# Kernel optimization log

Measured on AMD Instinct MI355X. Metric: run time of the kernel, lower is better.

The kernel has to match this reference:

```python
import jax, jax.numpy as jnp
import numpy as np

R = 3                 # corr_radius
STRIDE = 4
RES = (384, 512)      # model_resolution (H, W)
G = 2 * R + 1         # 7: support grid side


def setup_inputs() -> dict:
    key = jax.random.key(0)
    ks = jax.random.split(key, 16)
    B, S, N, C = 1, 8, 1024, 128
    H0, W0 = RES[0] // STRIDE, RES[1] // STRIDE  # 96, 128
    inp = {}
    for i in range(4):
        h, w = H0 >> i, W0 >> i
        inp[f"fmaps{i}"] = jax.random.normal(ks[i], (B, S, C, h, w), jnp.float32)
        inp[f"track{i}"] = jax.random.normal(ks[4 + i], (B, G * G, N, C), jnp.float32)
    inp["coords"] = jax.random.uniform(ks[8], (B, S, N, 2), jnp.float32) * jnp.asarray([W0 - 1.0, H0 - 1.0], jnp.float32)
    inp["vis"] = jax.random.normal(ks[9], (B, S, N, 1), jnp.float32)
    inp["conf"] = jax.random.normal(ks[10], (B, S, N, 1), jnp.float32)
    r2 = G * G
    inp["w1"] = jax.random.normal(ks[11], (r2 * r2, 384), jnp.float32) * (1.0 / np.sqrt(r2 * r2))
    inp["b1"] = jnp.zeros((384,), jnp.float32)
    inp["w2"] = jax.random.normal(ks[12], (384, 256), jnp.float32) * (1.0 / np.sqrt(384))
    inp["b2"] = jnp.zeros((256,), jnp.float32)
    inp["time_emb"] = jax.random.normal(ks[13], (1, S, 1110), jnp.float32) * 0.02
    return inp


def bilinear_sample(fmap, x, y):
    """fmap: (BT, C, H, W); x, y: (BT, M) pixel coords. Border padding, align_corners=True
    (matches torch grid_sample as used by co-tracker's bilinear_sampler)."""
    BT, C, H, W = fmap.shape
    x0f = jnp.floor(x)
    y0f = jnp.floor(y)
    wx = (x - x0f)[:, None, :]
    wy = (y - y0f)[:, None, :]
    x0 = jnp.clip(x0f.astype(jnp.int32), 0, W - 1)
    x1 = jnp.clip(x0f.astype(jnp.int32) + 1, 0, W - 1)
    y0 = jnp.clip(y0f.astype(jnp.int32), 0, H - 1)
    y1 = jnp.clip(y0f.astype(jnp.int32) + 1, 0, H - 1)
    flat = fmap.reshape(BT, C, H * W)

    def g(yi, xi):
        idx = (yi * W + xi)[:, None, :]  # (BT, 1, M)
        return jnp.take_along_axis(flat, idx, axis=2)  # (BT, C, M)

    return (g(y0, x0) * (1 - wx) * (1 - wy) + g(y0, x1) * wx * (1 - wy)
            + g(y1, x0) * (1 - wx) * wy + g(y1, x1) * wx * wy)


def posenc(x, min_deg=0, max_deg=10):
    scales = jnp.asarray([2.0 ** i for i in range(min_deg, max_deg)], x.dtype)
    xb = (x[..., None, :] * scales[:, None]).reshape(x.shape[:-1] + (-1,))
    four = jnp.sin(jnp.concatenate([xb, xb + 0.5 * jnp.pi], axis=-1))
    return jnp.concatenate([x, four], axis=-1)


def reference(fmaps0, fmaps1, fmaps2, fmaps3, track0, track1, track2, track3,
              coords, vis, conf, w1, b1, w2, b2, time_emb):
    B, S, N, _ = coords.shape
    fps = [fmaps0, fmaps1, fmaps2, fmaps3]
    tps = [track0, track1, track2, track3]
    d = jnp.linspace(-R, R, G)
    xoff, yoff = jnp.meshgrid(d, d, indexing='ij')  # (7,7): rows = x offset, cols = y offset

    embs = []
    for lvl in range(4):
        fm = fps[lvl]
        C, H, W = fm.shape[2], fm.shape[3], fm.shape[4]
        c = coords.reshape(B * S, N, 1, 1, 2) / (2.0 ** lvl)
        x = c[..., 0] + xoff          # (B*S, N, 7, 7)
        y = c[..., 1] + yoff
        M = N * G * G
        sampled = bilinear_sample(fm.reshape(B * S, C, H, W), x.reshape(B * S, M), y.reshape(B * S, M))
        corr_feat = sampled.reshape(B, S, C, N, G, G).transpose(0, 1, 3, 4, 5, 2)  # (B,S,N,7,7,C)
        track = tps[lvl].reshape(B, G, G, N, C).transpose(0, 3, 1, 2, 4)           # (B,N,7,7,C)
        vol = jnp.einsum('btnhwc,bnijc->btnhwij', corr_feat, track)                # (B,S,N,7,7,7,7)
        h = jax.nn.gelu(vol.reshape(B * S * N, G * G * G * G) @ w1 + b1, approximate=False)
        embs.append(h @ w2 + b2)
    corr_embs = jnp.concatenate(embs, axis=-1).reshape(B, S, N, -1)  # (B,S,N,1024)

    rel_f = jnp.pad(coords[:, :-1] - coords[:, 1:], ((0, 0), (0, 1), (0, 0), (0, 0)))
    rel_b = jnp.pad(coords[:, 1:] - coords[:, :-1], ((0, 0), (1, 0), (0, 0), (0, 0)))
    scale = jnp.asarray([RES[1], RES[0]], jnp.float32) / STRIDE
    rel_emb = posenc(jnp.concatenate([rel_f / scale, rel_b / scale], axis=-1))  # (B,S,N,84)

    x = jnp.concatenate([vis, conf, corr_embs, rel_emb], axis=-1)  # (B,S,N,1110)
    x = x.transpose(0, 2, 1, 3).reshape(B * N, S, -1) + time_emb
    return x.reshape(B, N, S, -1)
```

## Files before the change

kernel.cpp:

```cpp
#include <hip/hip_runtime.h>
#include <math.h>


#define SN 8
#define NN 1024
#define CC 128
#define K1P2 2752
#define H1 384
#define H2 256
#define DOUT 1110

typedef short bf16x8 __attribute__((ext_vector_type(8)));
typedef short s16x4 __attribute__((ext_vector_type(4)));
typedef float f32x4 __attribute__((ext_vector_type(4)));

__device__ inline unsigned short f2b(float x) {
    union { float f; unsigned u; } v; v.f = x;
    unsigned r = v.u + 0x7FFFu + ((v.u >> 16) & 1u);
    return (unsigned short)(r >> 16);
}
__device__ inline float b2f(unsigned short u) {
    union { unsigned u; float f; } v; v.u = (unsigned)u << 16; return v.f;
}
__device__ inline void gll16(const void* g, void* l) {
    __builtin_amdgcn_global_load_lds(
        (const __attribute__((address_space(1))) void*)g,
        (__attribute__((address_space(3))) void*)l, 16, 0, 0);
}
__device__ inline int swz(int row, int g) {
    return row * 128 + ((g ^ (row & 7)) << 3);
}

__global__ __launch_bounds__(256) void conv_fmap_kernel(
    const float* __restrict__ in, unsigned short* __restrict__ outp,
    int H, int W)
{
    const int Hp = H + 8, Wp = W + 8;
    const int s = blockIdx.x / Hp, yp = blockIdx.x % Hp;
    const int y = min(max(yp - 4, 0), H - 1);
    const float* src = in + (size_t)s * CC * H * W + (size_t)y * W;
    unsigned short* dst = outp + ((size_t)s * Hp + yp) * Wp * CC;
    for (int idx = threadIdx.x; idx < Wp * CC; idx += 256) {
        int xp = idx >> 7, c = idx & 127;
        int x = min(max(xp - 4, 0), W - 1);
        dst[idx] = f2b(src[(size_t)c * H * W + x]);
    }
}

__global__ __launch_bounds__(256, 3) void sample_vol_kernel(
    const unsigned short* __restrict__ fq0, const unsigned short* __restrict__ fq1,
    const unsigned short* __restrict__ fq2, const unsigned short* __restrict__ fq3,
    const float* __restrict__ tk0, const float* __restrict__ tk1,
    const float* __restrict__ tk2, const float* __restrict__ tk3,
    const float* __restrict__ coords,
    unsigned short* __restrict__ vol,
    int lv0)
{
    __shared__ __align__(16) unsigned short bufA[80 * 128];
    __shared__ __align__(16) unsigned short bufB[80 * 128];
    __shared__ __align__(16) unsigned short pcL[80 * 68];
    const int n = blockIdx.x & 1023, g = blockIdx.x >> 10;
    const int lvl = lv0 + g;
    const unsigned short* fpad = (lvl == 0) ? fq0 : (lvl == 1) ? fq1
                               : (lvl == 2) ? fq2 : fq3;
    const float* track = (lvl == 0) ? tk0 : (lvl == 1) ? tk1
                       : (lvl == 2) ? tk2 : tk3;
    const int Wp = (128 >> lvl) + 8;
    const int t = threadIdx.x;
    const int lane = t & 63, wv = t >> 6;
    const int rsub = lane & 15, kq = lane >> 4;
    const float inv = 1.0f / (float)(1 << lvl);
    const size_t plane = (size_t)((96 >> lvl) + 8) * Wp * CC;

    int poff[5], ldso[5];
    #pragma unroll
    for (int i = 0; i < 5; ++i) {
        int task64 = wv * 5 + i;
        int point = task64 * 4 + (lane >> 4);
        int v = point / 10, xs = point - v * 10;
        int j = (lane & 15) ^ (point & 7);
        poff[i] = (v * Wp + xs) * CC + j * 8;
        ldso[i] = task64 * 512;
    }

    float cxa[SN], cya[SN];
    int fxa[SN], fya[SN], ea[SN];
    #pragma unroll
    for (int s = 0; s < SN; ++s) {
        float2 c2 = *(const float2*)&coords[((size_t)s * NN + n) * 2];
        cxa[s] = c2.x * inv; cya[s] = c2.y * inv;
        fxa[s] = (int)floorf(cxa[s]);
        fya[s] = (int)floorf(cya[s]);
        ea[s] = (fxa[s] - 3) & ~1;
    }

    int p0b[2], ij0a[2], tau8[2]; bool vld[2];
    #pragma unroll
    for (int rep = 0; rep < 2; ++rep) {
        int tau = t + rep * 256;
        vld[rep] = (tau < 343);
        int tt = vld[rep] ? tau : 0;
        int ab = tt / 7, blk = tt - 7 * ab;
        int a = ab / 7, b = ab - 7 * a;
        p0b[rep] = b * 10 + a;
        ij0a[rep] = blk * 8;
        tau8[rep] = tt * 8;
    }

    {
        const unsigned short* base =
            fpad + ((fya[0] + 1) * Wp + (ea[0] + 4)) * CC;
        #pragma unroll
        for (int i = 0; i < 5; ++i) gll16(base + poff[i], &bufA[ldso[i]]);
    }
    for (int task = t; task < 49 * 16; task += 256) {
        int row = task >> 4, gg = task & 15;
        const float* srcp = &track[((size_t)row * NN + n) * CC + gg * 8];
        float4 f0 = *(const float4*)srcp;
        float4 f1 = *(const float4*)(srcp + 4);
        bf16x8 v8;
        v8[0] = f2b(f0.x); v8[1] = f2b(f0.y); v8[2] = f2b(f0.z); v8[3] = f2b(f0.w);
        v8[4] = f2b(f1.x); v8[5] = f2b(f1.y); v8[6] = f2b(f1.z); v8[7] = f2b(f1.w);
        *(bf16x8*)&bufB[swz(row, gg)] = v8;
    }
    {
        unsigned* T32 = (unsigned*)bufB;
        for (int i = t; i < 15 * 64; i += 256) T32[49 * 64 + i] = 0;
    }
    asm volatile("s_waitcnt lgkmcnt(0)" ::: "memory");
    __builtin_amdgcn_sched_barrier(0);
    __builtin_amdgcn_s_barrier();
    bf16x8 tf[4];
    #pragma unroll
    for (int kk = 0; kk < 4; ++kk)
        tf[kk] = *(const bf16x8*)&bufB[swz(wv * 16 + rsub, kk * 4 + kq)];
    asm volatile("s_waitcnt lgkmcnt(0)" ::: "memory");
    __builtin_amdgcn_sched_barrier(0);
    __builtin_amdgcn_s_barrier();
    __builtin_amdgcn_sched_barrier(0);
    {
        const unsigned short* base =
            fpad + plane + ((fya[1] + 1) * Wp + (ea[1] + 4)) * CC;
        #pragma unroll
        for (int i = 0; i < 5; ++i) gll16(base + poff[i], &bufB[ldso[i]]);
    }

    #pragma unroll
    for (int sl = 0; sl < SN; ++sl) {
        unsigned short* pbuf = (sl & 1) ? bufB : bufA;
        const float wx = cxa[sl] - (float)fxa[sl], wy = cya[sl] - (float)fya[sl];
        const float w00 = (1.f - wx) * (1.f - wy), w10 = wx * (1.f - wy);
        const float w01 = (1.f - wx) * wy,         w11 = wx * wy;
        const int off = fxa[sl] - 3 - ea[sl];

        if (sl == 0) {
            asm volatile("s_waitcnt vmcnt(5) lgkmcnt(0)" ::: "memory");
        } else if (sl == 1) {
            if (wv < 2) asm volatile("s_waitcnt vmcnt(7) lgkmcnt(0)" ::: "memory");
            else        asm volatile("s_waitcnt vmcnt(6) lgkmcnt(0)" ::: "memory");
        } else if (sl == SN - 1) {
            if (wv < 2) asm volatile("s_waitcnt vmcnt(4) lgkmcnt(0)" ::: "memory");
            else        asm volatile("s_waitcnt vmcnt(2) lgkmcnt(0)" ::: "memory");
        } else {
            if (wv < 2) asm volatile("s_waitcnt vmcnt(9) lgkmcnt(0)" ::: "memory");
            else        asm volatile("s_waitcnt vmcnt(7) lgkmcnt(0)" ::: "memory");
        }
        __builtin_amdgcn_sched_barrier(0);
        __builtin_amdgcn_s_barrier();
        __builtin_amdgcn_sched_barrier(0);

        {
            f32x4 acc[5] = {};
            __builtin_amdgcn_s_setprio(1);
            #pragma unroll
            for (int kk = 0; kk < 4; ++kk) {
                int gg = kk * 4 + kq;
                #pragma unroll
                for (int ti = 0; ti < 5; ++ti) {
                    bf16x8 a = *(const bf16x8*)&pbuf[swz(ti * 16 + rsub, gg)];
                    acc[ti] = __builtin_amdgcn_mfma_f32_16x16x32_bf16(a, tf[kk], acc[ti], 0, 0, 0);
                }
            }
            __builtin_amdgcn_s_setprio(0);
            const int col = wv * 16 + rsub;
            #pragma unroll
            for (int ti = 0; ti < 5; ++ti)
                #pragma unroll
                for (int r = 0; r < 4; ++r)
                    pcL[(ti * 16 + kq * 4 + r) * 68 + col] = f2b(acc[ti][r]);
        }
        asm volatile("s_waitcnt lgkmcnt(0)" ::: "memory");
        __builtin_amdgcn_s_barrier();
        __builtin_amdgcn_sched_barrier(0);

        if (sl + 2 < SN) {
            const unsigned short* base =
                fpad + (size_t)(sl + 2) * plane
                + ((fya[sl + 2] + 1) * Wp + (ea[sl + 2] + 4)) * CC;
            #pragma unroll
            for (int i = 0; i < 5; ++i) gll16(base + poff[i], &pbuf[ldso[i]]);
        }
        __builtin_amdgcn_sched_barrier(0);

        {
            unsigned short* vrow = vol + ((size_t)(g * SN + sl) * NN + n) * K1P2;
            #pragma unroll
            for (int rep = 0; rep < 2; ++rep) {
                if (vld[rep]) {
                    int base = (p0b[rep] + off) * 68 + ij0a[rep];
                    s16x4 a0 = *(const s16x4*)&pcL[base],       a1 = *(const s16x4*)&pcL[base + 4];
                    s16x4 b0 = *(const s16x4*)&pcL[base + 68],  b1 = *(const s16x4*)&pcL[base + 72];
                    s16x4 c0 = *(const s16x4*)&pcL[base + 680], c1 = *(const s16x4*)&pcL[base + 684];
                    s16x4 d0 = *(const s16x4*)&pcL[base + 748], d1 = *(const s16x4*)&pcL[base + 752];
                    unsigned w[4];
                    #pragma unroll
                    for (int j = 0; j < 4; ++j) {
                        const int e0 = 2 * j, e1 = 2 * j + 1;
                        float v0 = w00 * b2f((unsigned short)(e0 < 4 ? a0[e0 & 3] : a1[e0 & 3]))
                                 + w10 * b2f((unsigned short)(e0 < 4 ? b0[e0 & 3] : b1[e0 & 3]))
                                 + w01 * b2f((unsigned short)(e0 < 4 ? c0[e0 & 3] : c1[e0 & 3]))
                                 + w11 * b2f((unsigned short)(e0 < 4 ? d0[e0 & 3] : d1[e0 & 3]));
                        float v1 = w00 * b2f((unsigned short)(e1 < 4 ? a0[e1 & 3] : a1[e1 & 3]))
                                 + w10 * b2f((unsigned short)(e1 < 4 ? b0[e1 & 3] : b1[e1 & 3]))
                                 + w01 * b2f((unsigned short)(e1 < 4 ? c0[e1 & 3] : c1[e1 & 3]))
                                 + w11 * b2f((unsigned short)(e1 < 4 ? d0[e1 & 3] : d1[e1 & 3]));
                        w[j] = (unsigned)f2b(v0) | ((unsigned)f2b(v1) << 16);
                    }
                    uint4 st; st.x = w[0]; st.y = w[1]; st.z = w[2]; st.w = w[3];
                    *(uint4*)(vrow + tau8[rep]) = st;
                }
            }
        }
    }
}

__global__ __launch_bounds__(256) void zpad_kernel(
    unsigned short* __restrict__ vol, int rows)
{
    int r = blockIdx.x * 256 + threadIdx.x;
    if (r < rows) {
        uint4 z; z.x = 0; z.y = 0; z.z = 0; z.w = 0;
        *(uint4*)(vol + (size_t)r * K1P2 + 2744) = z;
    }
}

__global__ __launch_bounds__(256) void conv_w1_kernel(
    const float* __restrict__ w1, unsigned short* __restrict__ w1t)
{
    __shared__ float tile[32][33];
    const int kb = blockIdx.x * 32, nb = blockIdx.y * 32;
    const int tx = threadIdx.x & 31, ty = threadIdx.x >> 5;
    #pragma unroll
    for (int i = 0; i < 32; i += 8) {
        int kp = kb + ty + i;
        int k = -1;
        if (kp < 2744) {
            int tau = kp >> 3, r = kp & 7;
            int ab = tau / 7, blk = tau - 7 * ab;
            int ij = blk * 8 + r;
            if (ij < 49) k = ab * 49 + ij;
        }
        tile[ty + i][tx] = (k >= 0) ? w1[(size_t)k * H1 + nb + tx] : 0.f;
    }
    __syncthreads();
    #pragma unroll
    for (int i = 0; i < 32; i += 8)
        w1t[(size_t)(nb + ty + i) * K1P2 + kb + tx] = f2b(tile[tx][ty + i]);
}

__global__ __launch_bounds__(256, 3) void gemm1_kernel(
    const unsigned short* __restrict__ A,
    const unsigned short* __restrict__ Bt,
    const float* __restrict__ bias,
    unsigned short* __restrict__ Hout)
{
    __shared__ __align__(16) unsigned short As[3 * 128 * 32];
    __shared__ __align__(16) unsigned short Bs[3 * 128 * 32];
    const int h = blockIdx.x, q = gridDim.x >> 3;
    const int l = (h & 7) * q + (h >> 3);
    const int m0 = (l / 3) * 128, n0 = (l % 3) * 128;
    const int t = threadIdx.x, lane = t & 63, wv = t >> 6;
    const int wm = wv >> 1, wn = wv & 1;
    const int rsub = lane & 15, kq = lane >> 4;

    const int rA0 = t >> 2, sA0 = (t & 3) ^ ((rA0 >> 1) & 3);
    const int rA1 = (t + 256) >> 2, sA1 = ((t + 256) & 3) ^ ((rA1 >> 1) & 3);
    const unsigned short* gA0 = A  + (size_t)(m0 + rA0) * K1P2 + sA0 * 8;
    const unsigned short* gA1 = A  + (size_t)(m0 + rA1) * K1P2 + sA1 * 8;
    const unsigned short* gB0 = Bt + (size_t)(n0 + rA0) * K1P2 + sA0 * 8;
    const unsigned short* gB1 = Bt + (size_t)(n0 + rA1) * K1P2 + sA1 * 8;
    const int chunk0 = (t & ~63) * 8, chunk1 = (256 + (t & ~63)) * 8;

    f32x4 acc[4][4] = {};

    const int NSTEP = K1P2 / 32;
    #pragma unroll
    for (int p = 0; p < 3; ++p) {
        size_t ko = (size_t)p * 32;
        int lb = p * 4096;
        gll16(gA0 + ko, &As[lb + chunk0]); gll16(gA1 + ko, &As[lb + chunk1]);
        gll16(gB0 + ko, &Bs[lb + chunk0]); gll16(gB1 + ko, &Bs[lb + chunk1]);
    }
    int cur = 0;
    for (int st = 0; st < NSTEP; ++st) {
        const int rem = NSTEP - 1 - st;
        if (rem >= 2)      asm volatile("s_waitcnt vmcnt(8)" ::: "memory");
        else if (rem == 1) asm volatile("s_waitcnt vmcnt(4)" ::: "memory");
        else               asm volatile("s_waitcnt vmcnt(0)" ::: "memory");
        __builtin_amdgcn_s_barrier();
        __builtin_amdgcn_sched_barrier(0);
        const int lb = cur * 4096;
        bf16x8 af[4], bfr[4];
        #pragma unroll
        for (int mi = 0; mi < 4; ++mi) {
            int r = wm * 64 + mi * 16 + rsub;
            int phys = r * 4 + (kq ^ ((r >> 1) & 3));
            af[mi] = *(const bf16x8*)&As[lb + phys * 8];
        }
        #pragma unroll
        for (int ni = 0; ni < 4; ++ni) {
            int r = wn * 64 + ni * 16 + rsub;
            int phys = r * 4 + (kq ^ ((r >> 1) & 3));
            bfr[ni] = *(const bf16x8*)&Bs[lb + phys * 8];
        }
        __builtin_amdgcn_s_setprio(1);
        #pragma unroll
        for (int mi = 0; mi < 4; ++mi)
            #pragma unroll
            for (int ni = 0; ni < 4; ++ni)
                acc[mi][ni] = __builtin_amdgcn_mfma_f32_16x16x32_bf16(
                    af[mi], bfr[ni], acc[mi][ni], 0, 0, 0);
        __builtin_amdgcn_s_setprio(0);
        __builtin_amdgcn_sched_barrier(0);
        __builtin_amdgcn_s_barrier();
        __builtin_amdgcn_sched_barrier(0);
        if (st + 3 < NSTEP) {
            size_t ko = (size_t)(st + 3) * 32;
            gll16(gA0 + ko, &As[lb + chunk0]);
            gll16(gA1 + ko, &As[lb + chunk1]);
            gll16(gB0 + ko, &Bs[lb + chunk0]);
            gll16(gB1 + ko, &Bs[lb + chunk1]);
        }
        cur = (cur == 2) ? 0 : cur + 1;
    }
    #pragma unroll
    for (int mi = 0; mi < 4; ++mi) {
        int row = m0 + wm * 64 + mi * 16 + kq * 4;
        #pragma unroll
        for (int ni = 0; ni < 4; ++ni) {
            int col = n0 + wn * 64 + ni * 16 + rsub;
            float bcol = bias[col];
            #pragma unroll
            for (int r = 0; r < 4; ++r) {
                float x = acc[mi][ni][r] + bcol;
                float gg = 0.5f * x * (1.f + erff(x * 0.70710678118654752f));
                Hout[(size_t)(row + r) * H1 + col] = f2b(gg);
            }
        }
    }
}

__global__ __launch_bounds__(256, 3) void gemm2_kernel(
    const unsigned short* __restrict__ A,
    const unsigned short* __restrict__ Bt,
    const float* __restrict__ bias,
    const float* __restrict__ te,
    float* __restrict__ out,
    int lv0)
{
    __shared__ __align__(16) unsigned short As[3 * 128 * 32];
    __shared__ __align__(16) unsigned short Bs[3 * 128 * 32];
    const int h = blockIdx.x, q = gridDim.x >> 3;
    const int l = (h & 7) * q + (h >> 3);
    const int m0 = (l >> 1) * 128, n0 = (l & 1) * 128;
    const int t = threadIdx.x, lane = t & 63, wv = t >> 6;
    const int wm = wv >> 1, wn = wv & 1;
    const int rsub = lane & 15, kq = lane >> 4;

    const int rA0 = t >> 2, sA0 = (t & 3) ^ ((rA0 >> 1) & 3);
    const int rA1 = (t + 256) >> 2, sA1 = ((t + 256) & 3) ^ ((rA1 >> 1) & 3);
    const unsigned short* gA0 = A  + (size_t)(m0 + rA0) * H1 + sA0 * 8;
    const unsigned short* gA1 = A  + (size_t)(m0 + rA1) * H1 + sA1 * 8;
    const unsigned short* gB0 = Bt + (size_t)(n0 + rA0) * H1 + sA0 * 8;
    const unsigned short* gB1 = Bt + (size_t)(n0 + rA1) * H1 + sA1 * 8;
    const int chunk0 = (t & ~63) * 8, chunk1 = (256 + (t & ~63)) * 8;

    f32x4 acc[4][4] = {};

    const int NSTEP = H1 / 32;
    #pragma unroll
    for (int p = 0; p < 3; ++p) {
        size_t ko = (size_t)p * 32;
        int lb = p * 4096;
        gll16(gA0 + ko, &As[lb + chunk0]); gll16(gA1 + ko, &As[lb + chunk1]);
        gll16(gB0 + ko, &Bs[lb + chunk0]); gll16(gB1 + ko, &Bs[lb + chunk1]);
    }
    int cur = 0;
    for (int st = 0; st < NSTEP; ++st) {
        const int rem = NSTEP - 1 - st;
        if (rem >= 2)      asm volatile("s_waitcnt vmcnt(8)" ::: "memory");
        else if (rem == 1) asm volatile("s_waitcnt vmcnt(4)" ::: "memory");
        else               asm volatile("s_waitcnt vmcnt(0)" ::: "memory");
        __builtin_amdgcn_s_barrier();
        __builtin_amdgcn_sched_barrier(0);
        const int lb = cur * 4096;
        bf16x8 af[4], bfr[4];
        #pragma unroll
        for (int mi = 0; mi < 4; ++mi) {
            int r = wm * 64 + mi * 16 + rsub;
            int phys = r * 4 + (kq ^ ((r >> 1) & 3));
            af[mi] = *(const bf16x8*)&As[lb + phys * 8];
        }
        #pragma unroll
        for (int ni = 0; ni < 4; ++ni) {
            int r = wn * 64 + ni * 16 + rsub;
            int phys = r * 4 + (kq ^ ((r >> 1) & 3));
            bfr[ni] = *(const bf16x8*)&Bs[lb + phys * 8];
        }
        __builtin_amdgcn_s_setprio(1);
        #pragma unroll
        for (int mi = 0; mi < 4; ++mi)
            #pragma unroll
            for (int ni = 0; ni < 4; ++ni)
                acc[mi][ni] = __builtin_amdgcn_mfma_f32_16x16x32_bf16(
                    af[mi], bfr[ni], acc[mi][ni], 0, 0, 0);
        __builtin_amdgcn_s_setprio(0);
        __builtin_amdgcn_sched_barrier(0);
        __builtin_amdgcn_s_barrier();
        __builtin_amdgcn_sched_barrier(0);
        if (st + 3 < NSTEP) {
            size_t ko = (size_t)(st + 3) * 32;
            gll16(gA0 + ko, &As[lb + chunk0]);
            gll16(gA1 + ko, &As[lb + chunk1]);
            gll16(gB0 + ko, &Bs[lb + chunk0]);
            gll16(gB1 + ko, &Bs[lb + chunk1]);
        }
        cur = (cur == 2) ? 0 : cur + 1;
    }
    #pragma unroll
    for (int mi = 0; mi < 4; ++mi) {
        int rowb = m0 + wm * 64 + mi * 16 + kq * 4;
        #pragma unroll
        for (int ni = 0; ni < 4; ++ni) {
            int col = n0 + wn * 64 + ni * 16 + rsub;
            float bcol = bias[col];
            #pragma unroll
            for (int r = 0; r < 4; ++r) {
                int row = rowb + r;
                int g = row >> 13, s = (row >> 10) & 7, n = row & 1023;
                int dcol = 2 + (lv0 + g) * H2 + col;
                out[((size_t)n * SN + s) * DOUT + dcol] =
                    acc[mi][ni][r] + bcol + te[s * DOUT + dcol];
            }
        }
    }
}

__global__ __launch_bounds__(256) void conv_t_kernel(
    const float* __restrict__ in, unsigned short* __restrict__ outp,
    int K, int Nw, int Kp)
{
    __shared__ float tile[32][33];
    const int kb = blockIdx.x * 32, nb = blockIdx.y * 32;
    const int tx = threadIdx.x & 31, ty = threadIdx.x >> 5;
    #pragma unroll
    for (int i = 0; i < 32; i += 8) {
        int k = kb + ty + i, nn = nb + tx;
        tile[ty + i][tx] = (k < K && nn < Nw) ? in[(size_t)k * Nw + nn] : 0.f;
    }
    __syncthreads();
    #pragma unroll
    for (int i = 0; i < 32; i += 8) {
        int nn = nb + ty + i, k = kb + tx;
        if (nn < Nw) outp[(size_t)nn * Kp + k] = f2b(tile[tx][ty + i]);
    }
}

__global__ __launch_bounds__(128) void tail_kernel(
    const float* __restrict__ coords, const float* __restrict__ vis,
    const float* __restrict__ conf, const float* __restrict__ te,
    float* __restrict__ out)
{
    const int b = blockIdx.x;
    const int n = b >> 3, s = b & 7;
    const int d = threadIdx.x;
    if (d >= 86) return;
    const size_t ob = (size_t)b * DOUT;
    if (d == 0) {
        out[ob + 0] = vis[(size_t)s * NN + n] + te[s * DOUT + 0];
    } else if (d == 1) {
        out[ob + 1] = conf[(size_t)s * NN + n] + te[s * DOUT + 1];
    } else {
        int rd = d - 2;
        float cx = coords[((size_t)s * NN + n) * 2 + 0];
        float cy = coords[((size_t)s * NN + n) * 2 + 1];
        float rfx = 0.f, rfy = 0.f, rbx = 0.f, rby = 0.f;
        if (s < SN - 1) {
            rfx = cx - coords[((size_t)(s + 1) * NN + n) * 2 + 0];
            rfy = cy - coords[((size_t)(s + 1) * NN + n) * 2 + 1];
        }
        if (s > 0) {
            rbx = cx - coords[((size_t)(s - 1) * NN + n) * 2 + 0];
            rby = cy - coords[((size_t)(s - 1) * NN + n) * 2 + 1];
        }
        float r4[4] = {rfx / 128.f, rfy / 96.f, rbx / 128.f, rby / 96.f};
        float val;
        if (rd < 4) {
            val = r4[rd];
        } else if (rd < 44) {
            int q = rd - 4; int deg = q >> 2, comp = q & 3;
            val = sinf(r4[comp] * (float)(1 << deg));
        } else {
            int q = rd - 44; int deg = q >> 2, comp = q & 3;
            val = sinf(r4[comp] * (float)(1 << deg) + 1.57079632679489662f);
        }
        int od = 1026 + rd;
        out[ob + od] = val + te[s * DOUT + od];
    }
}

extern "C" void kernel_launch(void* const* d_in, const int* in_sizes, int n_in,
                              void* d_out, int out_size, void* d_ws, size_t ws_size,
                              hipStream_t stream) {
    const float* fmaps[4] = {(const float*)d_in[0], (const float*)d_in[2],
                             (const float*)d_in[4], (const float*)d_in[6]};
    const float* track[4] = {(const float*)d_in[1], (const float*)d_in[3],
                             (const float*)d_in[5], (const float*)d_in[7]};
    const float* coords = (const float*)d_in[8];
    const float* vis    = (const float*)d_in[9];
    const float* conf   = (const float*)d_in[10];
    const float* w1     = (const float*)d_in[11];
    const float* b1     = (const float*)d_in[12];
    const float* w2     = (const float*)d_in[13];
    const float* b2     = (const float*)d_in[14];
    const float* te     = (const float*)d_in[15];
    float* out = (float*)d_out;

    const int Hs[4] = {96, 48, 24, 12};
    const int Ws[4] = {128, 64, 32, 16};

    char* wsb = (char*)d_ws;
    unsigned short* w1t = (unsigned short*)wsb;
    size_t off = (size_t)H1 * K1P2 * 2;
    unsigned short* w2t = (unsigned short*)(wsb + off);
    off += (size_t)H2 * H1 * 2;
    unsigned short* fpad[4];
    for (int l = 0; l < 4; ++l) {
        fpad[l] = (unsigned short*)(wsb + off);
        off += (size_t)SN * (Hs[l] + 8) * (Ws[l] + 8) * CC * 2;
    }
    off += 512;
    const size_t fixed = off;
    int n_lv = 4;
    while (n_lv > 1 &&
           fixed + (size_t)n_lv * SN * NN * (K1P2 + H1) * 2 > ws_size)
        n_lv >>= 1;
    unsigned short* volb = (unsigned short*)(wsb + fixed);
    unsigned short* hb   = volb + (size_t)n_lv * SN * NN * K1P2;

    conv_w1_kernel<<<dim3(K1P2 / 32, H1 / 32), 256, 0, stream>>>(w1, w1t);
    conv_t_kernel<<<dim3(H1 / 32, H2 / 32), 256, 0, stream>>>(w2, w2t, H1, H2, H1);
    for (int l = 0; l < 4; ++l)
        conv_fmap_kernel<<<SN * (Hs[l] + 8), 256, 0, stream>>>(
            fmaps[l], fpad[l], Hs[l], Ws[l]);
    zpad_kernel<<<(n_lv * SN * NN + 255) / 256, 256, 0, stream>>>(
        volb, n_lv * SN * NN);

    for (int lv0 = 0; lv0 < 4; lv0 += n_lv) {
        sample_vol_kernel<<<n_lv * NN, 256, 0, stream>>>(
            fpad[0], fpad[1], fpad[2], fpad[3],
            track[0], track[1], track[2], track[3],
            coords, volb, lv0);
        const int rows = n_lv * SN * NN;
        gemm1_kernel<<<(rows / 128) * 3, 256, 0, stream>>>(volb, w1t, b1, hb);
        gemm2_kernel<<<(rows / 128) * 2, 256, 0, stream>>>(hb, w2t, b2, te, out, lv0);
    }
    tail_kernel<<<SN * NN, 128, 0, stream>>>(coords, vis, conf, te, out);
}
```

Measured before the change: 342.3 us.

## Widen gemm1 tile to full 384-column N per block with 512 threads

Each gemm1 block now covers a 128x384 output tile (all of H1) using 8 waves in a 2x4 arrangement, instead of three separate 128x128 blocks per row panel. The A panel (the large volume matrix) is therefore loaded from global memory once rather than three times, cutting the dominant memory traffic. The cost is more LDS per block (about 96KB across three stages), more accumulators per thread (24 MFMA tiles), a third as many blocks, and lower occupancy, which could limit latency hiding.

```diff
diff --git a/kernel.cpp b/kernel.cpp
--- a/kernel.cpp
+++ b/kernel.cpp
@@ -268,38 +268,44 @@
         w1t[(size_t)(nb + ty + i) * K1P2 + kb + tx] = f2b(tile[tx][ty + i]);
 }
 
-__global__ __launch_bounds__(256, 3) void gemm1_kernel(
+__global__ __launch_bounds__(512, 2) void gemm1_kernel(
     const unsigned short* __restrict__ A,
     const unsigned short* __restrict__ Bt,
     const float* __restrict__ bias,
     unsigned short* __restrict__ Hout)
 {
     __shared__ __align__(16) unsigned short As[3 * 128 * 32];
-    __shared__ __align__(16) unsigned short Bs[3 * 128 * 32];
+    __shared__ __align__(16) unsigned short Bs[3 * 384 * 32];
     const int h = blockIdx.x, q = gridDim.x >> 3;
     const int l = (h & 7) * q + (h >> 3);
-    const int m0 = (l / 3) * 128, n0 = (l % 3) * 128;
+    const int m0 = l * 128;
     const int t = threadIdx.x, lane = t & 63, wv = t >> 6;
-    const int wm = wv >> 1, wn = wv & 1;
+    const int wm = wv >> 2, wn = wv & 3;
     const int rsub = lane & 15, kq = lane >> 4;
 
-    const int rA0 = t >> 2, sA0 = (t & 3) ^ ((rA0 >> 1) & 3);
-    const int rA1 = (t + 256) >> 2, sA1 = ((t + 256) & 3) ^ ((rA1 >> 1) & 3);
-    const unsigned short* gA0 = A  + (size_t)(m0 + rA0) * K1P2 + sA0 * 8;
-    const unsigned short* gA1 = A  + (size_t)(m0 + rA1) * K1P2 + sA1 * 8;
-    const unsigned short* gB0 = Bt + (size_t)(n0 + rA0) * K1P2 + sA0 * 8;
-    const unsigned short* gB1 = Bt + (size_t)(n0 + rA1) * K1P2 + sA1 * 8;
-    const int chunk0 = (t & ~63) * 8, chunk1 = (256 + (t & ~63)) * 8;
-
-    f32x4 acc[4][4] = {};
+    const int rA = t >> 2, sA = (t & 3) ^ ((rA >> 1) & 3);
+    const unsigned short* gA = A + (size_t)(m0 + rA) * K1P2 + sA * 8;
+    const int chA = (t & ~63) * 8;
+    const unsigned short* gB[3];
+    int chB[3];
+    #pragma unroll
+    for (int j = 0; j < 3; ++j) {
+        int gg = t + 512 * j;
+        int rB = gg >> 2, sB = (gg & 3) ^ ((rB >> 1) & 3);
+        gB[j] = Bt + (size_t)rB * K1P2 + sB * 8;
+        chB[j] = (t & ~63) * 8 + j * 4096;
+    }
+
+    f32x4 acc[4][6] = {};
 
     const int NSTEP = K1P2 / 32;
     #pragma unroll
     for (int p = 0; p < 3; ++p) {
         size_t ko = (size_t)p * 32;
-        int lb = p * 4096;
-        gll16(gA0 + ko, &As[lb + chunk0]); gll16(gA1 + ko, &As[lb + chunk1]);
-        gll16(gB0 + ko, &Bs[lb + chunk0]); gll16(gB1 + ko, &Bs[lb + chunk1]);
+        gll16(gA + ko, &As[p * 4096 + chA]);
+        #pragma unroll
+        for (int j = 0; j < 3; ++j)
+            gll16(gB[j] + ko, &Bs[p * 12288 + chB[j]]);
     }
     int cur = 0;
     for (int st = 0; st < NSTEP; ++st) {
@@ -309,25 +315,25 @@
         else               asm volatile("s_waitcnt vmcnt(0)" ::: "memory");
         __builtin_amdgcn_s_barrier();
         __builtin_amdgcn_sched_barrier(0);
-        const int lb = cur * 4096;
-        bf16x8 af[4], bfr[4];
+        const int lbA = cur * 4096, lbB = cur * 12288;
+        bf16x8 af[4], bfr[6];
         #pragma unroll
         for (int mi = 0; mi < 4; ++mi) {
             int r = wm * 64 + mi * 16 + rsub;
             int phys = r * 4 + (kq ^ ((r >> 1) & 3));
-            af[mi] = *(const bf16x8*)&As[lb + phys * 8];
-        }
-        #pragma unroll
-        for (int ni = 0; ni < 4; ++ni) {
-            int r = wn * 64 + ni * 16 + rsub;
+            af[mi] = *(const bf16x8*)&As[lbA + phys * 8];
+        }
+        #pragma unroll
+        for (int ni = 0; ni < 6; ++ni) {
+            int r = wn * 96 + ni * 16 + rsub;
             int phys = r * 4 + (kq ^ ((r >> 1) & 3));
-            bfr[ni] = *(const bf16x8*)&Bs[lb + phys * 8];
+            bfr[ni] = *(const bf16x8*)&Bs[lbB + phys * 8];
         }
         __builtin_amdgcn_s_setprio(1);
         #pragma unroll
         for (int mi = 0; mi < 4; ++mi)
             #pragma unroll
-            for (int ni = 0; ni < 4; ++ni)
+            for (int ni = 0; ni < 6; ++ni)
                 acc[mi][ni] = __builtin_amdgcn_mfma_f32_16x16x32_bf16(
                     af[mi], bfr[ni], acc[mi][ni], 0, 0, 0);
         __builtin_amdgcn_s_setprio(0);
@@ -336,10 +342,10 @@
         __builtin_amdgcn_sched_barrier(0);
         if (st + 3 < NSTEP) {
             size_t ko = (size_t)(st + 3) * 32;
-            gll16(gA0 + ko, &As[lb + chunk0]);
-            gll16(gA1 + ko, &As[lb + chunk1]);
-            gll16(gB0 + ko, &Bs[lb + chunk0]);
-            gll16(gB1 + ko, &Bs[lb + chunk1]);
+            gll16(gA + ko, &As[lbA + chA]);
+            #pragma unroll
+            for (int j = 0; j < 3; ++j)
+                gll16(gB[j] + ko, &Bs[lbB + chB[j]]);
         }
         cur = (cur == 2) ? 0 : cur + 1;
     }
@@ -347,8 +353,8 @@
     for (int mi = 0; mi < 4; ++mi) {
         int row = m0 + wm * 64 + mi * 16 + kq * 4;
         #pragma unroll
-        for (int ni = 0; ni < 4; ++ni) {
-            int col = n0 + wn * 64 + ni * 16 + rsub;
+        for (int ni = 0; ni < 6; ++ni) {
+            int col = wn * 96 + ni * 16 + rsub;
             float bcol = bias[col];
             #pragma unroll
             for (int r = 0; r < 4; ++r) {
@@ -572,7 +578,7 @@
             track[0], track[1], track[2], track[3],
             coords, volb, lv0);
         const int rows = n_lv * SN * NN;
-        gemm1_kernel<<<(rows / 128) * 3, 256, 0, stream>>>(volb, w1t, b1, hb);
+        gemm1_kernel<<<rows / 128, 512, 0, stream>>>(volb, w1t, b1, hb);
         gemm2_kernel<<<(rows / 128) * 2, 256, 0, stream>>>(hb, w2t, b2, te, out, lv0);
     }
     tail_kernel<<<SN * NN, 128, 0, stream>>>(coords, vis, conf, te, out);
```

After: 374.7 us. 1.09x slower.
